# Kernel tuning notes

Measured on AMD Instinct MI355X. Metric: run time of the kernel, lower is better.

Reference implementation:

```python
import jax, jax.numpy as jnp
import numpy as np

B, C, T = 32, 64, 512
K = 3            # period_channels / top-k frequencies
PMAX = T         # max period (== seq_len so output matches input length)
MIN_P = 32       # min_period_threshold
CMAX = T // MIN_P  # static upper bound on number of cycles
KERNELS = ((1, 1), (3, 3), (5, 5))


def _conv2d(x, w, b, pad):
    # x: [N, Cin, H, W], w: [Cout, Cin, kh, kw]
    y = jax.lax.conv_general_dilated(
        x, w, (1, 1), ((pad[0], pad[0]), (pad[1], pad[1])),
        dimension_numbers=('NCHW', 'OIHW', 'NCHW'))
    return y + b[None, :, None, None]


def _period_fold(seqs):
    # seqs: [BN, T]. FFT top-k period detection + gather-based fold into 2D grids.
    spec = jnp.fft.rfft(seqs, axis=-1)
    amp = jnp.abs(spec).at[..., 0].set(0.0)  # zero DC component
    vals, idx = jax.lax.top_k(amp, K)        # [BN, K]
    idx = jnp.maximum(idx, 1)
    P = jnp.clip(T // idx, MIN_P, PMAX)      # period length per branch
    cycles = jnp.maximum(T // P, 1)
    base = jnp.maximum(T - cycles * P, 0)    # start offset (keep trailing window)
    idx_c = jnp.arange(CMAX)
    idx_p = jnp.arange(PMAX)
    gidx = (base[:, :, None, None]
            + idx_c[None, None, :, None] * P[:, :, None, None]
            + idx_p[None, None, None, :])
    gidx = jnp.clip(gidx, 0, T - 1)          # [BN, K, CMAX, PMAX]
    gathered = seqs[jnp.arange(seqs.shape[0])[:, None, None, None], gidx]
    mask = ((idx_c[None, None, :, None] < cycles[:, :, None, None])
            & (idx_p[None, None, None, :] < P[:, :, None, None])).astype(seqs.dtype)
    return gathered * mask, mask, vals


def _forward(features, w_path0, b_path0, w_path1, b_path1, w_path2, b_path2,
             w_proj, b_proj, w_res, b_res, w_fuse, b_fuse):
    seqs = features.reshape(B * C, T)
    conv_in, mask, kamp = _period_fold(seqs)  # [B*C, K, CMAX, PMAX]
    # Inception block: parallel same-padded convs + 1x1 proj + residual 1x1 proj
    ws = (w_path0, w_path1, w_path2)
    bs = (b_path0, b_path1, b_path2)
    feats = [_conv2d(conv_in, w, b, (kh // 2, kw // 2))
             for w, b, (kh, kw) in zip(ws, bs, KERNELS)]
    z = _conv2d(jnp.concatenate(feats, axis=1), w_proj, b_proj, (0, 0))
    z = jax.nn.gelu(z, approximate=False)  # torch nn.GELU default = exact erf
    z2d = (z + _conv2d(conv_in, w_res, b_res, (0, 0))).reshape(B, C, CMAX, PMAX)
    mask5 = mask.reshape(B, C, K, CMAX, PMAX)
    conv_in5 = conv_in.reshape(B, C, K, CMAX, PMAX)
    eps = jnp.finfo(z2d.dtype).eps
    neg = jnp.finfo(z2d.dtype).min
    # masked avg / max pooling over cycles
    cycle_mask = mask5.max(axis=2)                       # [B,C,CMAX,PMAX]
    avg_pool = (z2d * cycle_mask).sum(axis=2) / (cycle_mask.sum(axis=2) + eps)
    valid = cycle_mask > 0
    max_pool = jnp.where(valid, z2d, neg).max(axis=2)
    max_pool = jnp.where(valid.any(axis=2), max_pool, 0.0)  # [B,C,PMAX]
    # amplitude-softmax weighted branch reconstruction back to 1D
    branch_sum = conv_in5.sum(axis=3)                    # [B,C,K,PMAX]
    branch_w = mask5.sum(axis=3)
    branch_recon = branch_sum / (branch_w + eps) * (branch_w > 0)
    branch_valid = mask5.max(axis=(3, 4)) > 0            # [B,C,K]
    amp = jnp.where(branch_valid, kamp.reshape(B, C, K), neg)
    bw = jax.nn.softmax(amp, axis=2) * branch_valid
    seq_recon = (branch_recon * bw[..., None]).sum(axis=2)  # [B,C,PMAX]
    combined = jnp.concatenate([avg_pool, max_pool, seq_recon], axis=1)  # [B,3C,PMAX]
    fused = jnp.einsum('oc,bct->bot', w_fuse, combined) + b_fuse[None, :, None]
    return jax.nn.gelu(fused, approximate=False)  # [B, C, T] residual update


def setup_inputs() -> dict:
    key = jax.random.key(0)
    ks = jax.random.split(key, 8)

    def conv_w(k, shape):
        fan_in = shape[1] * shape[2] * shape[3]
        return jax.random.normal(k, shape, jnp.float32) / float(np.sqrt(fan_in))

    inp = {'features': jax.random.normal(ks[0], (B, C, T), jnp.float32)}
    for i, (kh, kw) in enumerate(KERNELS):
        inp[f'w_path{i}'] = conv_w(ks[1 + i], (1, K, kh, kw))
        inp[f'b_path{i}'] = jnp.zeros((1,), jnp.float32)
    inp['w_proj'] = conv_w(ks[4], (1, len(KERNELS), 1, 1))
    inp['b_proj'] = jnp.zeros((1,), jnp.float32)
    inp['w_res'] = conv_w(ks[5], (1, K, 1, 1))
    inp['b_res'] = jnp.zeros((1,), jnp.float32)
    inp['w_fuse'] = jax.random.normal(ks[6], (C, 3 * C), jnp.float32) / float(np.sqrt(3 * C))
    inp['b_fuse'] = jnp.zeros((C,), jnp.float32)
    return inp


def reference(features, w_path0, b_path0, w_path1, b_path1, w_path2, b_path2,
              w_proj, b_proj, w_res, b_res, w_fuse, b_fuse):
    return _forward(features, w_path0, b_path0, w_path1, b_path1, w_path2, b_path2,
                    w_proj, b_proj, w_res, b_res, w_fuse, b_fuse)
```

## Files before the change

### kernel.cpp

```cpp
#include <hip/hip_runtime.h>
#include <math.h>

#define B_    32
#define C_    64
#define T_    512
#define NROWS (B_ * C_)
#define CMAX_ 16
#define FEPS  1.1920929e-07f

__device__ __forceinline__ float gelu_fast(float x) {
    float y = fmaf(0.044715f * x * x, x, x);
    float e = __builtin_exp2f(-2.3022808f * y);
    return x * __builtin_amdgcn_rcpf(1.0f + e);
}

__global__ __launch_bounds__(128) void mono_kernel(
    const float* __restrict__ feat,
    const float* __restrict__ w0, const float* __restrict__ b0,
    const float* __restrict__ w1, const float* __restrict__ b1,
    const float* __restrict__ w2, const float* __restrict__ b2,
    const float* __restrict__ wpj, const float* __restrict__ bpj,
    const float* __restrict__ wr, const float* __restrict__ br,
    float* __restrict__ avg_out, float* __restrict__ max_out,
    float* __restrict__ seq_out)
{
    __shared__ float rowp[1040];
    __shared__ __align__(16) float2 FA[256];
    __shared__ __align__(16) float2 FB[256];
    __shared__ float WeffS[80];
    __shared__ float WsumS[25];
    __shared__ float wtopS[6];
    __shared__ int   itopS[6];
    __shared__ int   ipS[9];
    __shared__ float bwS[3];

    const int tid = threadIdx.x;
    const int lane = tid & 63;
    const int wv = tid >> 6;
    const int r = blockIdx.x;

    {
        float4 v = reinterpret_cast<const float4*>(feat + (size_t)r * T_)[tid];
        int bi = 2 + tid * 4;
        rowp[bi + 0] = v.x; rowp[bi + 1] = v.y;
        rowp[bi + 2] = v.z; rowp[bi + 3] = v.w;
    }
    for (int i = 514 + tid; i < 1040; i += 128) rowp[i] = 0.f;
    if (tid == 0) { rowp[0] = 0.f; rowp[1] = 0.f; }
    if (tid < 80) {
        int i = tid;
        if (i < 75) {
            int k = i / 25, ij = i % 25, ii = ij / 5, jj = ij % 5;
            float w = wpj[2] * w2[k * 25 + ii * 5 + jj];
            if (ii >= 1 && ii <= 3 && jj >= 1 && jj <= 3)
                w += wpj[1] * w1[k * 9 + (ii - 1) * 3 + (jj - 1)];
            if (ii == 2 && jj == 2) w += wpj[0] * w0[k];
            WeffS[i] = w;
        } else if (i == 75) {
            WeffS[75] = wpj[0] * b0[0] + wpj[1] * b1[0] + wpj[2] * b2[0] + bpj[0];
        } else if (i <= 78) {
            WeffS[i] = wr[i - 76];
        } else {
            WeffS[79] = br[0];
        }
    }
    __syncthreads();

    {
        float2* Fw = FA + (wv << 7);
        #pragma unroll
        for (int n = lane; n < 128; n += 64)
            Fw[n] = make_float2(rowp[2 + 4 * n + 2 * wv], rowp[3 + 4 * n + 2 * wv]);
    }

    {
        float2* src = FA + (wv << 7);
        float2* dst = FB + (wv << 7);
        #pragma unroll
        for (int s = 1; s <= 7; ++s) {
            const int l = 1 << (s - 1);
            const int pl = lane & (l - 1);
            const int i0 = 2 * lane - pl;
            const float rev = (float)pl * (0.5f / (float)l);
            const float cw =  __builtin_amdgcn_cosf(rev);
            const float sw = -__builtin_amdgcn_sinf(rev);
            float2 a = src[lane];
            float2 b = src[lane + 64];
            float tr = cw * b.x - sw * b.y;
            float ti = cw * b.y + sw * b.x;
            dst[i0]     = make_float2(a.x + tr, a.y + ti);
            dst[i0 + l] = make_float2(a.x - tr, a.y - ti);
            float2* tmp = src; src = dst; dst = tmp;
        }
    }
    __syncthreads();

    float v[2]; int id[2];
    {
        const float2* Fe = FB;
        const float2* Fo = FB + 128;
        const int k1 = tid + 1;
        const int a = k1 & 127;
        const int b = (128 - a) & 127;
        float2 Fea = Fe[a], Foa = Fo[a], Feb = Fe[b], Fob = Fo[b];
        const float revw = (float)k1 * (1.0f / 256.0f);
        const float cw =  __builtin_amdgcn_cosf(revw);
        const float sw = -__builtin_amdgcn_sinf(revw);
        float wfr = cw * Foa.x - sw * Foa.y, wfi = cw * Foa.y + sw * Foa.x;
        float cfr = cw * Fob.x + sw * Fob.y, cfi = cw * Fob.y - sw * Fob.x;
        const float revu = (float)k1 * (1.0f / 512.0f);
        const float su = __builtin_amdgcn_sinf(revu);
        const float cu = __builtin_amdgcn_cosf(revu);
        #pragma unroll
        for (int q = 0; q < 2; ++q) {
            const float sgn = q ? -1.f : 1.f;
            float Ax = Fea.x + sgn * wfr, Ay = Fea.y + sgn * wfi;
            float Bx = Feb.x + sgn * cfr, By = Feb.y + sgn * cfi;
            float Er = 0.5f * (Ax + Bx);
            float Ei = 0.5f * (Ay - By);
            float Or = 0.5f * (Ay + By);
            float Oi = 0.5f * (Bx - Ax);
            float cth = q ? -su : cu;
            float sth = q ?  cu : su;
            float Fr = Er + cth * Or + sth * Oi;
            float Fi = Ei + cth * Oi - sth * Or;
            v[q] = sqrtf(Fr * Fr + Fi * Fi);
            id[q] = k1 + 128 * q;
        }
    }

    {
        float vals[3]; int idxs[3];
        #pragma unroll
        for (int kk = 0; kk < 3; ++kk) {
            float bv = v[0]; int bi = id[0];
            if (v[1] > bv || (v[1] == bv && id[1] < bi)) { bv = v[1]; bi = id[1]; }
            #pragma unroll
            for (int off = 32; off >= 1; off >>= 1) {
                float ov = __shfl_xor(bv, off, 64);
                int   oi = __shfl_xor(bi, off, 64);
                if (ov > bv || (ov == bv && oi < bi)) { bv = ov; bi = oi; }
            }
            vals[kk] = bv; idxs[kk] = bi;
            #pragma unroll
            for (int q = 0; q < 2; ++q)
                if (id[q] == bi) v[q] = -1e30f;
        }
        if (lane == 0) {
            #pragma unroll
            for (int kk = 0; kk < 3; ++kk) {
                wtopS[wv * 3 + kk] = vals[kk];
                itopS[wv * 3 + kk] = idxs[kk];
            }
        }
    }
    if (tid < 25) WsumS[tid] = WeffS[tid] + WeffS[25 + tid] + WeffS[50 + tid];
    __syncthreads();
    if (tid == 0) {
        float vv[6]; int ii[6];
        #pragma unroll
        for (int q = 0; q < 6; ++q) { vv[q] = wtopS[q]; ii[q] = itopS[q]; }
        float vals[3]; int idxs[3];
        #pragma unroll
        for (int kk = 0; kk < 3; ++kk) {
            float bv = vv[0]; int bi = ii[0];
            #pragma unroll
            for (int q = 1; q < 6; ++q)
                if (vv[q] > bv || (vv[q] == bv && ii[q] < bi)) { bv = vv[q]; bi = ii[q]; }
            vals[kk] = bv; idxs[kk] = bi;
            #pragma unroll
            for (int q = 0; q < 6; ++q)
                if (ii[q] == bi) vv[q] = -1e30f;
        }
        float m = fmaxf(vals[0], fmaxf(vals[1], vals[2]));
        float e0 = expf(vals[0] - m), e1 = expf(vals[1] - m), e2 = expf(vals[2] - m);
        float inv = 1.0f / (e0 + e1 + e2);
        bwS[0] = e0 * inv; bwS[1] = e1 * inv; bwS[2] = e2 * inv;
        #pragma unroll
        for (int kk = 0; kk < 3; ++kk) {
            int fi = idxs[kk];
            int P = T_ / fi;
            P = P < 32 ? 32 : (P > 512 ? 512 : P);
            int cyc = T_ / P;
            ipS[kk] = P; ipS[3 + kk] = cyc; ipS[6 + kk] = T_ - cyc * P;
        }
    }
    __syncthreads();

    const int P0  = __builtin_amdgcn_readfirstlane(ipS[0]);
    const int P1  = __builtin_amdgcn_readfirstlane(ipS[1]);
    const int P2  = __builtin_amdgcn_readfirstlane(ipS[2]);
    const int cy0 = __builtin_amdgcn_readfirstlane(ipS[3]);
    const int cy1 = __builtin_amdgcn_readfirstlane(ipS[4]);
    const int cy2 = __builtin_amdgcn_readfirstlane(ipS[5]);
    const int bs0 = __builtin_amdgcn_readfirstlane(ipS[6]);
    const int bs1 = __builtin_amdgcn_readfirstlane(ipS[7]);
    const int bs2 = __builtin_amdgcn_readfirstlane(ipS[8]);
    const float bw0 = bwS[0], bw1 = bwS[1], bw2 = bwS[2];
    const float beff = WeffS[75], wr0 = WeffS[76], wr1 = WeffS[77],
                wr2 = WeffS[78], bres = WeffS[79];

    int maxP = P0 > P1 ? P0 : P1; maxP = maxP > P2 ? maxP : P2;
    const bool fastp = (P0 == P1) && (P1 == P2);
    const int kcount = fastp ? 1 : 3;
    const int PkA[3]  = {P0, P1, P2};
    const int cykA[3] = {cy0, cy1, cy2};
    const int bskA[3] = {bs0, bs1, bs2};
    const int woff = tid & 64;

    #pragma unroll 1
    for (int pc = 0; pc < T_; pc += 128) {
        const int p = pc + tid;
        const int wb = __builtin_amdgcn_readfirstlane(pc + woff);
        if (wb >= maxP) {
            avg_out[r * T_ + p] = 0.f;
            max_out[r * T_ + p] = 0.f;
            seq_out[r * T_ + p] = 0.f;
            continue;
        }
        int c0 = (P0 > wb) ? cy0 : 0;
        int c1 = (P1 > wb) ? cy1 : 0;
        int c2 = (P2 > wb) ? cy2 : 0;
        int cymax = c0 > c1 ? c0 : c1; cymax = cymax > c2 ? cymax : c2;
        cymax = __builtin_amdgcn_readfirstlane(cymax);

        float zacc[CMAX_];
        #pragma unroll
        for (int i = 0; i < CMAX_; ++i) zacc[i] = beff;

        #pragma unroll 1
        for (int k = 0; k < kcount; ++k) {
            const int P = PkA[k];
            if (wb >= P) continue;
            const int cy = cykA[k];
            const int bs = bskA[k];
            const float* Wsrc = fastp ? WsumS : (WeffS + k * 25);
            float Wk[5][5];
            #pragma unroll
            for (int i = 0; i < 5; ++i)
                #pragma unroll
                for (int j = 0; j < 5; ++j)
                    Wk[i][j] = Wsrc[i * 5 + j];
            bool mdw[5];
            #pragma unroll
            for (int dw = -2; dw <= 2; ++dw)
                mdw[dw + 2] = ((unsigned)(p + dw) < (unsigned)P);
            const int base = bs + p;
            #pragma unroll
            for (int g = 0; g < 4; ++g) {
                if (4 * g < cy) {
                    #pragma unroll
                    for (int h4 = 0; h4 < 4; ++h4) {
                        const int hh = 4 * g + h4;
                        const int hoff = (hh < cy) ? 0 : 4096;
                        int a0 = base + hh * P + hoff;
                        a0 = a0 > 1031 ? 1031 : a0;
                        float w[5];
                        #pragma unroll
                        for (int dw = 0; dw < 5; ++dw)
                            w[dw] = mdw[dw] ? rowp[a0 + dw] : 0.f;
                        #pragma unroll
                        for (int dh = -2; dh <= 2; ++dh) {
                            const int cc = hh - dh;
                            if (cc >= 0 && cc < CMAX_) {
                                #pragma unroll
                                for (int dw = 0; dw < 5; ++dw)
                                    zacc[cc] = fmaf(Wk[dh + 2][dw], w[dw], zacc[cc]);
                            }
                        }
                    }
                }
            }
        }

        float avg_num = 0.f, den = 0.f, mx = -3.402823466e38f;
        float s0 = 0.f, s1 = 0.f, s2 = 0.f;
        int anyv = 0;
        const int pl0 = (p < P0), pl1 = (p < P1), pl2 = (p < P2);
        #pragma unroll
        for (int cg = 0; cg < 4; ++cg) {
            if (4 * cg < cymax) {
                #pragma unroll
                for (int c4 = 0; c4 < 4; ++c4) {
                    const int cc = 4 * cg + c4;
                    int m0 = (cc < cy0) & pl0;
                    int m1 = (cc < cy1) & pl1;
                    int m2 = (cc < cy2) & pl2;
                    int a0 = 2 + bs0 + cc * P0 + p; a0 = a0 > 1036 ? 1036 : a0;
                    int a1 = 2 + bs1 + cc * P1 + p; a1 = a1 > 1036 ? 1036 : a1;
                    int a2 = 2 + bs2 + cc * P2 + p; a2 = a2 > 1036 ? 1036 : a2;
                    float x0v = m0 ? rowp[a0] : 0.f;
                    float x1v = m1 ? rowp[a1] : 0.f;
                    float x2v = m2 ? rowp[a2] : 0.f;
                    float res = fmaf(wr0, x0v, fmaf(wr1, x1v, fmaf(wr2, x2v, bres)));
                    float z = gelu_fast(zacc[cc]) + res;
                    s0 += x0v; s1 += x1v; s2 += x2v;
                    int mm = m0 | m1 | m2;
                    float cm = mm ? 1.f : 0.f;
                    avg_num += z * cm;
                    den += cm;
                    mx = mm ? fmaxf(mx, z) : mx;
                    anyv |= mm;
                }
            }
        }
        float avg = avg_num / (den + FEPS);
        float mpool = anyv ? mx : 0.f;

        float seq = 0.f;
        seq = fmaf(bw0, pl0 ? s0 / ((float)cy0 + FEPS) : 0.f, seq);
        seq = fmaf(bw1, pl1 ? s1 / ((float)cy1 + FEPS) : 0.f, seq);
        seq = fmaf(bw2, pl2 ? s2 / ((float)cy2 + FEPS) : 0.f, seq);

        avg_out[r * T_ + p] = avg;
        max_out[r * T_ + p] = mpool;
        seq_out[r * T_ + p] = seq;
    }
}

__global__ __launch_bounds__(256) void fuse_kernel(
    const float* __restrict__ avgb, const float* __restrict__ maxb,
    const float* __restrict__ seqb,
    const float* __restrict__ wf, const float* __restrict__ bfu,
    float* __restrict__ out)
{
    __shared__ float wT[64][70];
    __shared__ float Bt[64][40];
    const int tid = threadIdx.x;
    const int b = blockIdx.y;
    const int tt0 = blockIdx.x * 32;
    const int og = tid >> 3;
    const int tg = tid & 7;
    const int o0 = og * 2;
    const int t0 = tg * 4;

    float acc[2][4];
    #pragma unroll
    for (int i = 0; i < 2; ++i)
        #pragma unroll
        for (int j = 0; j < 4; ++j) acc[i][j] = 0.f;

    const float* srcs[3] = {avgb, maxb, seqb};
    for (int g = 0; g < 3; ++g) {
        const float* __restrict__ src = srcs[g];
        #pragma unroll
        for (int it = 0; it < 2; ++it) {
            int idx = tid + it * 256;
            int c = idx >> 3, t4 = idx & 7;
            float4 vv = reinterpret_cast<const float4*>(
                            &src[(b * 64 + c) * 512 + tt0])[t4];
            *reinterpret_cast<float4*>(&Bt[c][t4 * 4]) = vv;
        }
        #pragma unroll
        for (int it = 0; it < 16; ++it) {
            int i = tid + it * 256;
            int c = i & 63, o = i >> 6;
            wT[c][o] = wf[o * 192 + g * 64 + c];
        }
        __syncthreads();
        for (int c = 0; c < 64; ++c) {
            float2 wv = *reinterpret_cast<const float2*>(&wT[c][o0]);
            float4 bv = *reinterpret_cast<const float4*>(&Bt[c][t0]);
            const float wa[2] = {wv.x, wv.y};
            const float ba[4] = {bv.x, bv.y, bv.z, bv.w};
            #pragma unroll
            for (int i = 0; i < 2; ++i)
                #pragma unroll
                for (int j = 0; j < 4; ++j)
                    acc[i][j] = fmaf(wa[i], ba[j], acc[i][j]);
        }
        __syncthreads();
    }
    #pragma unroll
    for (int i = 0; i < 2; ++i) {
        float bias = bfu[o0 + i];
        float4 o4;
        o4.x = gelu_fast(acc[i][0] + bias);
        o4.y = gelu_fast(acc[i][1] + bias);
        o4.z = gelu_fast(acc[i][2] + bias);
        o4.w = gelu_fast(acc[i][3] + bias);
        *reinterpret_cast<float4*>(
            &out[(b * 64 + (o0 + i)) * 512 + tt0 + t0]) = o4;
    }
}

extern "C" void kernel_launch(void* const* d_in, const int* in_sizes, int n_in,
                              void* d_out, int out_size, void* d_ws, size_t ws_size,
                              hipStream_t stream) {
    const float* feat = (const float*)d_in[0];
    const float* w0  = (const float*)d_in[1];
    const float* b0  = (const float*)d_in[2];
    const float* w1  = (const float*)d_in[3];
    const float* b1  = (const float*)d_in[4];
    const float* w2  = (const float*)d_in[5];
    const float* b2  = (const float*)d_in[6];
    const float* wpj = (const float*)d_in[7];
    const float* bpj = (const float*)d_in[8];
    const float* wr  = (const float*)d_in[9];
    const float* br  = (const float*)d_in[10];
    const float* wf  = (const float*)d_in[11];
    const float* bfu = (const float*)d_in[12];

    float* ws = (float*)d_ws;
    float* avgb = ws;
    float* maxb = ws + (size_t)NROWS * T_;
    float* seqb = ws + 2 * (size_t)NROWS * T_;

    mono_kernel<<<NROWS, 128, 0, stream>>>(feat, w0, b0, w1, b1, w2, b2,
                                           wpj, bpj, wr, br, avgb, maxb, seqb);
    fuse_kernel<<<dim3(16, 32), 256, 0, stream>>>(avgb, maxb, seqb, wf, bfu,
                                                  (float*)d_out);
}
```

Measured before the change: 39.72 us.

## Split conv cycles across two waves per position chunk with LDS merge

Each block now processes period positions in 64-wide chunks. The two waves split the cycle dimension: each computes 8 cycle rows of the 5x5 conv plus pooling partials. Wave 1 writes its partial sums, max and sequence sums to shared memory and wave 0 merges them and writes the outputs. The aim is to halve the per-thread accumulator registers and skip chunks beyond maxP, at the cost of two barriers per chunk, some redundant halo loads and a wave idling during the merge.

```diff
diff --git a/kernel.cpp b/kernel.cpp
--- a/kernel.cpp
+++ b/kernel.cpp
@@ -206,33 +206,24 @@
     const int PkA[3]  = {P0, P1, P2};
     const int cykA[3] = {cy0, cy1, cy2};
     const int bskA[3] = {bs0, bs1, bs2};
-    const int woff = tid & 64;
+    const int ccb = wv << 3;
+    const int nchunk = (maxP + 63) >> 6;
+    float* mrg = reinterpret_cast<float*>(FA);
+    const size_t rT = (size_t)r * T_;
 
     #pragma unroll 1
-    for (int pc = 0; pc < T_; pc += 128) {
-        const int p = pc + tid;
-        const int wb = __builtin_amdgcn_readfirstlane(pc + woff);
-        if (wb >= maxP) {
-            avg_out[r * T_ + p] = 0.f;
-            max_out[r * T_ + p] = 0.f;
-            seq_out[r * T_ + p] = 0.f;
-            continue;
-        }
-        int c0 = (P0 > wb) ? cy0 : 0;
-        int c1 = (P1 > wb) ? cy1 : 0;
-        int c2 = (P2 > wb) ? cy2 : 0;
-        int cymax = c0 > c1 ? c0 : c1; cymax = cymax > c2 ? cymax : c2;
-        cymax = __builtin_amdgcn_readfirstlane(cymax);
-
-        float zacc[CMAX_];
-        #pragma unroll
-        for (int i = 0; i < CMAX_; ++i) zacc[i] = beff;
+    for (int ch = 0; ch < nchunk; ++ch) {
+        const int p = (ch << 6) + lane;
+
+        float zacc[8];
+        #pragma unroll
+        for (int i = 0; i < 8; ++i) zacc[i] = beff;
 
         #pragma unroll 1
         for (int k = 0; k < kcount; ++k) {
             const int P = PkA[k];
-            if (wb >= P) continue;
             const int cy = cykA[k];
+            if (ccb - 2 >= cy) continue;
             const int bs = bskA[k];
             const float* Wsrc = fastp ? WsumS : (WeffS + k * 25);
             float Wk[5][5];
@@ -247,25 +238,26 @@
                 mdw[dw + 2] = ((unsigned)(p + dw) < (unsigned)P);
             const int base = bs + p;
             #pragma unroll
-            for (int g = 0; g < 4; ++g) {
-                if (4 * g < cy) {
+            for (int g = 0; g < 3; ++g) {
+                if (ccb - 2 + 4 * g < cy) {
                     #pragma unroll
                     for (int h4 = 0; h4 < 4; ++h4) {
-                        const int hh = 4 * g + h4;
-                        const int hoff = (hh < cy) ? 0 : 4096;
+                        const int hh = ccb - 2 + 4 * g + h4;
+                        const bool vh = (unsigned)hh < (unsigned)cy;
+                        const int hoff = vh ? 0 : 4096;
                         int a0 = base + hh * P + hoff;
-                        a0 = a0 > 1031 ? 1031 : a0;
+                        a0 = a0 < 0 ? 0 : (a0 > 1031 ? 1031 : a0);
                         float w[5];
                         #pragma unroll
                         for (int dw = 0; dw < 5; ++dw)
                             w[dw] = mdw[dw] ? rowp[a0 + dw] : 0.f;
                         #pragma unroll
                         for (int dh = -2; dh <= 2; ++dh) {
-                            const int cc = hh - dh;
-                            if (cc >= 0 && cc < CMAX_) {
+                            const int cl = (4 * g + h4 - 2) - dh;
+                            if (cl >= 0 && cl < 8) {
                                 #pragma unroll
                                 for (int dw = 0; dw < 5; ++dw)
-                                    zacc[cc] = fmaf(Wk[dh + 2][dw], w[dw], zacc[cc]);
+                                    zacc[cl] = fmaf(Wk[dh + 2][dw], w[dw], zacc[cl]);
                             }
                         }
                     }
@@ -273,16 +265,16 @@
             }
         }
 
-        float avg_num = 0.f, den = 0.f, mx = -3.402823466e38f;
+        int cymax = cy0 > cy1 ? cy0 : cy1; cymax = cymax > cy2 ? cymax : cy2;
+        float num = 0.f, den = 0.f, mx = -3.402823466e38f;
         float s0 = 0.f, s1 = 0.f, s2 = 0.f;
-        int anyv = 0;
         const int pl0 = (p < P0), pl1 = (p < P1), pl2 = (p < P2);
         #pragma unroll
-        for (int cg = 0; cg < 4; ++cg) {
-            if (4 * cg < cymax) {
+        for (int cg = 0; cg < 2; ++cg) {
+            if (ccb + 4 * cg < cymax) {
                 #pragma unroll
                 for (int c4 = 0; c4 < 4; ++c4) {
-                    const int cc = 4 * cg + c4;
+                    const int cc = ccb + 4 * cg + c4;
                     int m0 = (cc < cy0) & pl0;
                     int m1 = (cc < cy1) & pl1;
                     int m2 = (cc < cy2) & pl2;
@@ -293,28 +285,47 @@
                     float x1v = m1 ? rowp[a1] : 0.f;
                     float x2v = m2 ? rowp[a2] : 0.f;
                     float res = fmaf(wr0, x0v, fmaf(wr1, x1v, fmaf(wr2, x2v, bres)));
-                    float z = gelu_fast(zacc[cc]) + res;
+                    float z = gelu_fast(zacc[4 * cg + c4]) + res;
                     s0 += x0v; s1 += x1v; s2 += x2v;
                     int mm = m0 | m1 | m2;
                     float cm = mm ? 1.f : 0.f;
-                    avg_num += z * cm;
+                    num += z * cm;
                     den += cm;
                     mx = mm ? fmaxf(mx, z) : mx;
-                    anyv |= mm;
                 }
             }
         }
-        float avg = avg_num / (den + FEPS);
-        float mpool = anyv ? mx : 0.f;
-
-        float seq = 0.f;
-        seq = fmaf(bw0, pl0 ? s0 / ((float)cy0 + FEPS) : 0.f, seq);
-        seq = fmaf(bw1, pl1 ? s1 / ((float)cy1 + FEPS) : 0.f, seq);
-        seq = fmaf(bw2, pl2 ? s2 / ((float)cy2 + FEPS) : 0.f, seq);
-
-        avg_out[r * T_ + p] = avg;
-        max_out[r * T_ + p] = mpool;
-        seq_out[r * T_ + p] = seq;
+
+        if (wv == 1) {
+            mrg[lane]       = num;  mrg[64 + lane]  = den;
+            mrg[128 + lane] = mx;   mrg[192 + lane] = s0;
+            mrg[256 + lane] = s1;   mrg[320 + lane] = s2;
+        }
+        __syncthreads();
+        if (wv == 0) {
+            num += mrg[lane];
+            den += mrg[64 + lane];
+            mx = fmaxf(mx, mrg[128 + lane]);
+            s0 += mrg[192 + lane];
+            s1 += mrg[256 + lane];
+            s2 += mrg[320 + lane];
+            float avg = num / (den + FEPS);
+            float mpool = (den > 0.f) ? mx : 0.f;
+            float seq = 0.f;
+            seq = fmaf(bw0, pl0 ? s0 / ((float)cy0 + FEPS) : 0.f, seq);
+            seq = fmaf(bw1, pl1 ? s1 / ((float)cy1 + FEPS) : 0.f, seq);
+            seq = fmaf(bw2, pl2 ? s2 / ((float)cy2 + FEPS) : 0.f, seq);
+            avg_out[rT + p] = avg;
+            max_out[rT + p] = mpool;
+            seq_out[rT + p] = seq;
+        }
+        __syncthreads();
+    }
+
+    for (int i = (nchunk << 6) + tid; i < T_; i += 128) {
+        avg_out[rT + i] = 0.f;
+        max_out[rT + i] = 0.f;
+        seq_out[rT + i] = 0.f;
     }
 }
 
```

After: 68.13 us. +71.5%, slower.
